# Optimization experiments

Hardware: AMD Instinct MI355X
Metric: run time of the kernel (lower is better)

## Reference

```python
import jax, jax.numpy as jnp
import numpy as np

FT_SIZE = 512
NUM_BUCKETS = 8
HID = 32
IN_FEATS = 770

def _crelu(x):
    return jnp.clip(x, 0.0, 1.0)

def setup_inputs() -> dict:
    key = jax.random.key(0)
    ks = jax.random.split(key, 8)
    B = 65536
    x = jax.random.uniform(ks[0], (B, 2 * IN_FEATS), dtype=jnp.float32)
    s = 0.05
    ft_w = jax.random.normal(ks[1], (FT_SIZE, IN_FEATS), dtype=jnp.float32) * s
    ft_b = jax.random.normal(ks[2], (FT_SIZE,), dtype=jnp.float32) * s
    h1_w = jax.random.normal(ks[3], (NUM_BUCKETS, HID, 2 * FT_SIZE), dtype=jnp.float32) * s
    h1_b = jax.random.normal(ks[4], (NUM_BUCKETS, HID), dtype=jnp.float32) * s
    h2_w = jax.random.normal(ks[5], (NUM_BUCKETS, HID, HID), dtype=jnp.float32) * s
    h2_b = jax.random.normal(ks[6], (NUM_BUCKETS, HID), dtype=jnp.float32) * s
    h3_w = jax.random.normal(ks[7], (NUM_BUCKETS, 1, HID), dtype=jnp.float32) * s
    h3_b = jnp.zeros((NUM_BUCKETS, 1), dtype=jnp.float32)
    return {"x": x, "ft_w": ft_w, "ft_b": ft_b, "h1_w": h1_w, "h1_b": h1_b,
            "h2_w": h2_w, "h2_b": h2_b, "h3_w": h3_w, "h3_b": h3_b}

def reference(x, ft_w, ft_b, h1_w, h1_b, h2_w, h2_b, h3_w, h3_b):
    stm = x[:, :IN_FEATS]          # [B, 770]
    nstm = x[:, IN_FEATS:]         # [B, 770]
    stm_ft = _crelu(stm @ ft_w.T + ft_b)    # [B, FT]
    nstm_ft = _crelu(nstm @ ft_w.T + ft_b)  # [B, FT]
    combined = jnp.concatenate([stm_ft, nstm_ft], axis=1)  # [B, 2FT]
    # bucket index from piece count (STM first 768 channels)
    pc = jnp.sum(x[:, :768], axis=1)
    bucket_idx = jnp.clip((pc * NUM_BUCKETS / 33.0).astype(jnp.int32), 0, NUM_BUCKETS - 1)  # [B]
    # compute all bucket heads (dense compute-all, matching original loop+stack)
    h = _crelu(jnp.einsum('bi,koi->bko', combined, h1_w) + h1_b)  # [B, K, 32]
    h = _crelu(jnp.einsum('bko,kpo->bkp', h, h2_w) + h2_b)        # [B, K, 32]
    all_out = jnp.einsum('bko,kpo->bkp', h, h3_w) + h3_b          # [B, K, 1]
    out = jnp.take_along_axis(all_out, bucket_idx[:, None, None], axis=1)  # [B,1,1]
    return out[:, 0, :]  # [B, 1]
```

## Files before the change

kernel.cpp:

```cpp
#include <hip/hip_runtime.h>
#include <hip/hip_bf16.h>
#include <stdint.h>


#define INF 770
#define KP  800
#define FT  512
#define K2  1024
#define N2  256

typedef _Float16 half8 __attribute__((ext_vector_type(8)));
typedef float floatx4 __attribute__((ext_vector_type(4)));

__device__ __forceinline__ float crelu_f(float v) {
    return v < 0.f ? 0.f : (v > 1.f ? 1.f : v);
}

__device__ __forceinline__ void gl_lds16(const _Float16* g, _Float16* l) {
    __builtin_amdgcn_global_load_lds(
        (__attribute__((address_space(1))) void*)(uintptr_t)(const void*)g,
        (__attribute__((address_space(3))) void*)l,
        16, 0, 0);
}

__global__ __launch_bounds__(256) void convert_x_kernel(
    const float* __restrict__ x, _Float16* __restrict__ x16,
    int* __restrict__ bucket, int B)
{
    __shared__ float red[4];
    int b = blockIdx.x;
    int tid = threadIdx.x, lane = tid & 63, w = tid >> 6;
    const float* src = x + (size_t)b * (2 * INF);
    _Float16* d0 = x16 + (size_t)b * KP;
    _Float16* d1 = x16 + ((size_t)B + b) * KP;
    float s = 0.f;
    for (int i = tid; i < KP; i += 256) {
        float v0 = 0.f, v1 = 0.f;
        if (i < INF) { v0 = src[i]; v1 = src[INF + i]; }
        d0[i] = (_Float16)v0;
        d1[i] = (_Float16)v1;
        if (i < 768) s += v0;
    }
    #pragma unroll
    for (int off = 32; off; off >>= 1) s += __shfl_down(s, off, 64);
    if (lane == 0) red[w] = s;
    __syncthreads();
    if (tid == 0) {
        float pc = red[0] + red[1] + red[2] + red[3];
        int bk = (int)(pc * (8.0f / 33.0f));
        bucket[b] = bk < 0 ? 0 : (bk > 7 ? 7 : bk);
    }
}

__global__ __launch_bounds__(256) void convert_w_kernel(
    const float* __restrict__ ftw, const float* __restrict__ h1w,
    _Float16* __restrict__ ftw16, _Float16* __restrict__ h1w16)
{
    int idx = blockIdx.x * 256 + threadIdx.x;
    const int FTW = FT * KP;
    if (idx < FTW) {
        int r = idx / KP, c = idx - r * KP;
        ftw16[idx] = (_Float16)(c < INF ? ftw[r * INF + c] : 0.f);
    } else {
        int j = idx - FTW;
        if (j < N2 * K2) h1w16[j] = (_Float16)h1w[j];
    }
}

__global__ __launch_bounds__(256) void gemm_ft_kernel(
    const _Float16* __restrict__ A,
    const _Float16* __restrict__ Bt,
    const float* __restrict__ bias,
    _Float16* __restrict__ C)
{
    __shared__ _Float16 lsA[128 * 32];
    __shared__ _Float16 lsB[128 * 32];
    int bid = blockIdx.x;
    int mt = bid >> 2, nt = bid & 3;
    int m0 = mt * 128, n0 = nt * 128;
    int tid = threadIdx.x, lane = tid & 63, w = tid >> 6;
    int rm = (w & 1) * 64, rn = (w >> 1) * 64;
    int colL = lane & 15, rowQ = lane >> 4;

    floatx4 acc[4][4] = {};

    for (int kt = 0; kt < KP / 32; ++kt) {
        int ks = kt * 32;
        #pragma unroll
        for (int p = 0; p < 2; ++p) {
            int qb = p * 256 + w * 64;
            int q = qb + lane;
            int r = q >> 2, c8 = q & 3;
            gl_lds16(A + (size_t)(m0 + r) * KP + ks + c8 * 8, lsA + qb * 8);
            gl_lds16(Bt + (size_t)(n0 + r) * KP + ks + c8 * 8, lsB + qb * 8);
        }
        asm volatile("s_waitcnt vmcnt(0)" ::: "memory");
        __syncthreads();

        half8 af[4], bf[4];
        #pragma unroll
        for (int i = 0; i < 4; ++i)
            af[i] = *(const half8*)(lsA + (rm + i * 16 + colL) * 32 + rowQ * 8);
        #pragma unroll
        for (int j = 0; j < 4; ++j)
            bf[j] = *(const half8*)(lsB + (rn + j * 16 + colL) * 32 + rowQ * 8);
        #pragma unroll
        for (int i = 0; i < 4; ++i)
            #pragma unroll
            for (int j = 0; j < 4; ++j)
                acc[i][j] = __builtin_amdgcn_mfma_f32_16x16x32_f16(af[i], bf[j], acc[i][j], 0, 0, 0);
        __syncthreads();
    }

    #pragma unroll
    for (int j = 0; j < 4; ++j) {
        int gn = n0 + rn + j * 16 + colL;
        float bv = bias[gn];
        #pragma unroll
        for (int i = 0; i < 4; ++i) {
            #pragma unroll
            for (int r = 0; r < 4; ++r) {
                int gm = m0 + rm + i * 16 + rowQ * 4 + r;
                float v = crelu_f(acc[i][j][r] + bv);
                C[(size_t)gm * FT + gn] = (_Float16)v;
            }
        }
    }
}

__global__ __launch_bounds__(256) void gemm_h1_kernel(
    const _Float16* __restrict__ C1,
    const _Float16* __restrict__ Bt,
    const float* __restrict__ bias,
    float* __restrict__ H,
    int B)
{
    __shared__ _Float16 lsA[128 * 32];
    __shared__ _Float16 lsB[128 * 32];
    int bid = blockIdx.x;
    int mt = bid >> 1, nt = bid & 1;
    int m0 = mt * 128, n0 = nt * 128;
    int tid = threadIdx.x, lane = tid & 63, w = tid >> 6;
    int rm = (w & 1) * 64, rn = (w >> 1) * 64;
    int colL = lane & 15, rowQ = lane >> 4;

    floatx4 acc[4][4] = {};

    for (int kt = 0; kt < K2 / 32; ++kt) {
        int ks = kt * 32;
        const _Float16* Abase = (ks < FT) ? (C1 + ks)
                                          : (C1 + (size_t)B * FT + (ks - FT));
        #pragma unroll
        for (int p = 0; p < 2; ++p) {
            int qb = p * 256 + w * 64;
            int q = qb + lane;
            int r = q >> 2, c8 = q & 3;
            gl_lds16(Abase + (size_t)(m0 + r) * FT + c8 * 8, lsA + qb * 8);
            gl_lds16(Bt + (size_t)(n0 + r) * K2 + ks + c8 * 8, lsB + qb * 8);
        }
        asm volatile("s_waitcnt vmcnt(0)" ::: "memory");
        __syncthreads();

        half8 af[4], bf[4];
        #pragma unroll
        for (int i = 0; i < 4; ++i)
            af[i] = *(const half8*)(lsA + (rm + i * 16 + colL) * 32 + rowQ * 8);
        #pragma unroll
        for (int j = 0; j < 4; ++j)
            bf[j] = *(const half8*)(lsB + (rn + j * 16 + colL) * 32 + rowQ * 8);
        #pragma unroll
        for (int i = 0; i < 4; ++i)
            #pragma unroll
            for (int j = 0; j < 4; ++j)
                acc[i][j] = __builtin_amdgcn_mfma_f32_16x16x32_f16(af[i], bf[j], acc[i][j], 0, 0, 0);
        __syncthreads();
    }

    #pragma unroll
    for (int j = 0; j < 4; ++j) {
        int gn = n0 + rn + j * 16 + colL;
        float bv = bias[gn];
        #pragma unroll
        for (int i = 0; i < 4; ++i) {
            #pragma unroll
            for (int r = 0; r < 4; ++r) {
                int gm = m0 + rm + i * 16 + rowQ * 4 + r;
                H[(size_t)gm * N2 + gn] = crelu_f(acc[i][j][r] + bv);
            }
        }
    }
}

__global__ __launch_bounds__(256) void tail_kernel(
    const float* __restrict__ H,
    const int* __restrict__ bucket,
    const float* __restrict__ h2w,
    const float* __restrict__ h2b,
    const float* __restrict__ h3w,
    const float* __restrict__ h3b,
    float* __restrict__ out, int B)
{
    int s = blockIdx.x * 8 + (threadIdx.x >> 5);
    int j = threadIdx.x & 31;
    if (s >= B) return;
    int k = bucket[s];
    float h1v = H[(size_t)s * N2 + k * 32 + j];
    const float* w2 = h2w + ((k * 32 + j) * 32);
    float a = h2b[k * 32 + j];
    #pragma unroll
    for (int i = 0; i < 32; ++i) a += w2[i] * __shfl(h1v, i, 32);
    a = crelu_f(a);
    float p = a * h3w[k * 32 + j];
    #pragma unroll
    for (int off = 16; off; off >>= 1) p += __shfl_down(p, off, 32);
    if (j == 0) out[s] = p + h3b[k];
}

extern "C" void kernel_launch(void* const* d_in, const int* in_sizes, int n_in,
                              void* d_out, int out_size, void* d_ws, size_t ws_size,
                              hipStream_t stream) {
    const float* x    = (const float*)d_in[0];
    const float* ftw  = (const float*)d_in[1];
    const float* ftb  = (const float*)d_in[2];
    const float* h1w  = (const float*)d_in[3];
    const float* h1b  = (const float*)d_in[4];
    const float* h2w  = (const float*)d_in[5];
    const float* h2b  = (const float*)d_in[6];
    const float* h3w  = (const float*)d_in[7];
    const float* h3b  = (const float*)d_in[8];
    float* out = (float*)d_out;

    int B = in_sizes[0] / (2 * INF);

    char* ws = (char*)d_ws;
    _Float16* x16   = (_Float16*)ws;
    size_t x16_b    = (size_t)2 * B * KP * sizeof(_Float16);
    _Float16* C1    = (_Float16*)(ws + x16_b);
    size_t c1_b     = (size_t)2 * B * FT * sizeof(_Float16);
    _Float16* ftw16 = (_Float16*)(ws + x16_b + c1_b);
    _Float16* h1w16 = ftw16 + (size_t)FT * KP;
    int* bucket     = (int*)(h1w16 + (size_t)N2 * K2);
    float* H        = (float*)ws;

    {
        int total = FT * KP + N2 * K2;
        convert_w_kernel<<<(total + 255) / 256, 256, 0, stream>>>(ftw, h1w, ftw16, h1w16);
    }
    convert_x_kernel<<<B, 256, 0, stream>>>(x, x16, bucket, B);
    {
        int grid = (2 * B / 128) * 4;
        gemm_ft_kernel<<<grid, 256, 0, stream>>>(x16, ftw16, ftb, C1);
    }
    {
        int grid = (B / 128) * 2;
        gemm_h1_kernel<<<grid, 256, 0, stream>>>(C1, h1w16, h1b, H, B);
    }
    tail_kernel<<<(B + 7) / 8, 256, 0, stream>>>(H, bucket, h2w, h2b, h3w, h3b, out, B);
}
```

Baseline: 898.2 us.

## Restructure FT and H1 GEMMs with LDS-resident B, register-prefetched A, XCD-aware mapping

```diff
diff --git a/kernel.cpp b/kernel.cpp
--- a/kernel.cpp
+++ b/kernel.cpp
@@ -3,14 +3,17 @@
 #include <stdint.h>
 
 
-#define INF 770
-#define KP  800
-#define FT  512
-#define K2  1024
-#define N2  256
+#define INF  770
+#define XROW 1540
+#define KP   800
+#define FT   512
+#define K2   1024
+#define N2   256
 
 typedef _Float16 half8 __attribute__((ext_vector_type(8)));
+typedef _Float16 half4 __attribute__((ext_vector_type(4)));
 typedef float floatx4 __attribute__((ext_vector_type(4)));
+typedef float floatx2 __attribute__((ext_vector_type(2)));
 
 __device__ __forceinline__ float crelu_f(float v) {
     return v < 0.f ? 0.f : (v > 1.f ? 1.f : v);
@@ -30,16 +33,30 @@
     __shared__ float red[4];
     int b = blockIdx.x;
     int tid = threadIdx.x, lane = tid & 63, w = tid >> 6;
-    const float* src = x + (size_t)b * (2 * INF);
-    _Float16* d0 = x16 + (size_t)b * KP;
-    _Float16* d1 = x16 + ((size_t)B + b) * KP;
+    const float* src = x + (size_t)b * XROW;
     float s = 0.f;
-    for (int i = tid; i < KP; i += 256) {
-        float v0 = 0.f, v1 = 0.f;
-        if (i < INF) { v0 = src[i]; v1 = src[INF + i]; }
-        d0[i] = (_Float16)v0;
-        d1[i] = (_Float16)v1;
-        if (i < 768) s += v0;
+    if (tid < 200) {
+        int i0 = tid * 4;
+        half4 v0, v1;
+        if (tid < 192) {
+            floatx4 f = *(const floatx4*)(src + i0);
+            v0[0] = (_Float16)f.x; v0[1] = (_Float16)f.y;
+            v0[2] = (_Float16)f.z; v0[3] = (_Float16)f.w;
+            s = (f.x + f.y) + (f.z + f.w);
+            floatx2 g0 = *(const floatx2*)(src + 770 + i0);
+            floatx2 g1 = *(const floatx2*)(src + 772 + i0);
+            v1[0] = (_Float16)g0.x; v1[1] = (_Float16)g0.y;
+            v1[2] = (_Float16)g1.x; v1[3] = (_Float16)g1.y;
+        } else if (tid == 192) {
+            floatx2 f = *(const floatx2*)(src + 768);
+            v0[0] = (_Float16)f.x; v0[1] = (_Float16)f.y; v0[2] = 0; v0[3] = 0;
+            floatx2 g = *(const floatx2*)(src + 1538);
+            v1[0] = (_Float16)g.x; v1[1] = (_Float16)g.y; v1[2] = 0; v1[3] = 0;
+        } else {
+            v0 = half4{0, 0, 0, 0}; v1 = half4{0, 0, 0, 0};
+        }
+        *(half4*)(x16 + (size_t)b * KP + i0) = v0;
+        *(half4*)(x16 + ((size_t)B + b) * KP + i0) = v1;
     }
     #pragma unroll
     for (int off = 32; off; off >>= 1) s += __shfl_down(s, off, 64);
@@ -47,7 +64,7 @@
     __syncthreads();
     if (tid == 0) {
         float pc = red[0] + red[1] + red[2] + red[3];
-        int bk = (int)(pc * (8.0f / 33.0f));
+        int bk = (int)((pc * 8.0f) / 33.0f);
         bucket[b] = bk < 0 ? 0 : (bk > 7 ? 7 : bk);
     }
 }
@@ -67,127 +84,170 @@
     }
 }
 
-__global__ __launch_bounds__(256) void gemm_ft_kernel(
+__global__ __launch_bounds__(256) void gemm_ft(
     const _Float16* __restrict__ A,
     const _Float16* __restrict__ Bt,
     const float* __restrict__ bias,
     _Float16* __restrict__ C)
 {
-    __shared__ _Float16 lsA[128 * 32];
-    __shared__ _Float16 lsB[128 * 32];
+    __shared__ _Float16 lsB[13 * 64 * 32];
     int bid = blockIdx.x;
-    int mt = bid >> 2, nt = bid & 3;
-    int m0 = mt * 128, n0 = nt * 128;
+    int xcd = bid & 7, kk = bid >> 3;
+    int mt = xcd * 64 + (kk >> 3), nt = kk & 7;
+    int m0 = mt * 256, n0 = nt * 64;
     int tid = threadIdx.x, lane = tid & 63, w = tid >> 6;
-    int rm = (w & 1) * 64, rn = (w >> 1) * 64;
     int colL = lane & 15, rowQ = lane >> 4;
+    int chA = rowQ ^ ((colL >> 1) & 3);
+    int mw = m0 + w * 64;
+
+    const _Float16* a0 = A + (size_t)(mw + colL) * KP + rowQ * 8;
 
     floatx4 acc[4][4] = {};
-
-    for (int kt = 0; kt < KP / 32; ++kt) {
-        int ks = kt * 32;
-        #pragma unroll
-        for (int p = 0; p < 2; ++p) {
-            int qb = p * 256 + w * 64;
-            int q = qb + lane;
-            int r = q >> 2, c8 = q & 3;
-            gl_lds16(A + (size_t)(m0 + r) * KP + ks + c8 * 8, lsA + qb * 8);
-            gl_lds16(Bt + (size_t)(n0 + r) * KP + ks + c8 * 8, lsB + qb * 8);
-        }
-        asm volatile("s_waitcnt vmcnt(0)" ::: "memory");
-        __syncthreads();
-
-        half8 af[4], bf[4];
-        #pragma unroll
-        for (int i = 0; i < 4; ++i)
-            af[i] = *(const half8*)(lsA + (rm + i * 16 + colL) * 32 + rowQ * 8);
+    half8 apf[3][4];
+
+    for (int t = tid; t < 13 * 256; t += 256) {
+        int ktb = t >> 8, r = t & 255, n = r >> 2, kq = r & 3;
+        int srcq = kq ^ ((n >> 1) & 3);
+        gl_lds16(Bt + (size_t)(n0 + n) * KP + ktb * 32 + srcq * 8, lsB + t * 8);
+    }
+    #pragma unroll
+    for (int d = 0; d < 3; ++d)
+        #pragma unroll
+        for (int i = 0; i < 4; ++i)
+            apf[d][i] = *(const half8*)(a0 + (size_t)i * 16 * KP + d * 32);
+    asm volatile("s_waitcnt vmcnt(0)" ::: "memory");
+    __syncthreads();
+
+    #pragma unroll
+    for (int kt = 0; kt < 25; ++kt) {
+        if (kt == 13) {
+            __syncthreads();
+            for (int t = tid; t < 12 * 256; t += 256) {
+                int ktb = t >> 8, r = t & 255, n = r >> 2, kq = r & 3;
+                int srcq = kq ^ ((n >> 1) & 3);
+                gl_lds16(Bt + (size_t)(n0 + n) * KP + (13 + ktb) * 32 + srcq * 8,
+                         lsB + t * 8);
+            }
+            asm volatile("s_waitcnt vmcnt(0)" ::: "memory");
+            __syncthreads();
+        }
+        int ktRel = (kt < 13) ? kt : kt - 13;
+        half8 bf[4], af[4];
         #pragma unroll
         for (int j = 0; j < 4; ++j)
-            bf[j] = *(const half8*)(lsB + (rn + j * 16 + colL) * 32 + rowQ * 8);
+            bf[j] = *(const half8*)(lsB + ktRel * 2048 + (j * 16 + colL) * 32 + chA * 8);
+        #pragma unroll
+        for (int i = 0; i < 4; ++i) af[i] = apf[kt % 3][i];
+        if (kt + 3 < 25) {
+            #pragma unroll
+            for (int i = 0; i < 4; ++i)
+                apf[kt % 3][i] = *(const half8*)(a0 + (size_t)i * 16 * KP + (kt + 3) * 32);
+        }
         #pragma unroll
         for (int i = 0; i < 4; ++i)
             #pragma unroll
             for (int j = 0; j < 4; ++j)
                 acc[i][j] = __builtin_amdgcn_mfma_f32_16x16x32_f16(af[i], bf[j], acc[i][j], 0, 0, 0);
-        __syncthreads();
     }
 
     #pragma unroll
     for (int j = 0; j < 4; ++j) {
-        int gn = n0 + rn + j * 16 + colL;
+        int gn = n0 + j * 16 + colL;
         float bv = bias[gn];
         #pragma unroll
-        for (int i = 0; i < 4; ++i) {
+        for (int i = 0; i < 4; ++i)
             #pragma unroll
             for (int r = 0; r < 4; ++r) {
-                int gm = m0 + rm + i * 16 + rowQ * 4 + r;
-                float v = crelu_f(acc[i][j][r] + bv);
-                C[(size_t)gm * FT + gn] = (_Float16)v;
+                int gm = mw + i * 16 + rowQ * 4 + r;
+                C[(size_t)gm * FT + gn] = (_Float16)crelu_f(acc[i][j][r] + bv);
             }
-        }
-    }
-}
-
-__global__ __launch_bounds__(256) void gemm_h1_kernel(
+    }
+}
+
+__global__ __launch_bounds__(256) void gemm_h1(
     const _Float16* __restrict__ C1,
     const _Float16* __restrict__ Bt,
     const float* __restrict__ bias,
     float* __restrict__ H,
     int B)
 {
-    __shared__ _Float16 lsA[128 * 32];
-    __shared__ _Float16 lsB[128 * 32];
+    __shared__ _Float16 lsB[13 * 64 * 32];
     int bid = blockIdx.x;
-    int mt = bid >> 1, nt = bid & 1;
-    int m0 = mt * 128, n0 = nt * 128;
+    int xcd = bid & 7, kk = bid >> 3;
+    int mt = xcd * 32 + (kk >> 2), nt = kk & 3;
+    int m0 = mt * 256, n0 = nt * 64;
     int tid = threadIdx.x, lane = tid & 63, w = tid >> 6;
-    int rm = (w & 1) * 64, rn = (w >> 1) * 64;
     int colL = lane & 15, rowQ = lane >> 4;
+    int chA = rowQ ^ ((colL >> 1) & 3);
+    int mw = m0 + w * 64;
+
+    const _Float16* a0lo = C1 + (size_t)(mw + colL) * FT + rowQ * 8;
+    const _Float16* a0hi = C1 + (size_t)(B + mw + colL) * FT + rowQ * 8;
 
     floatx4 acc[4][4] = {};
-
-    for (int kt = 0; kt < K2 / 32; ++kt) {
-        int ks = kt * 32;
-        const _Float16* Abase = (ks < FT) ? (C1 + ks)
-                                          : (C1 + (size_t)B * FT + (ks - FT));
-        #pragma unroll
-        for (int p = 0; p < 2; ++p) {
-            int qb = p * 256 + w * 64;
-            int q = qb + lane;
-            int r = q >> 2, c8 = q & 3;
-            gl_lds16(Abase + (size_t)(m0 + r) * FT + c8 * 8, lsA + qb * 8);
-            gl_lds16(Bt + (size_t)(n0 + r) * K2 + ks + c8 * 8, lsB + qb * 8);
-        }
-        asm volatile("s_waitcnt vmcnt(0)" ::: "memory");
-        __syncthreads();
-
-        half8 af[4], bf[4];
-        #pragma unroll
-        for (int i = 0; i < 4; ++i)
-            af[i] = *(const half8*)(lsA + (rm + i * 16 + colL) * 32 + rowQ * 8);
+    half8 apf[3][4];
+
+    #define H1_AFRAG(KT, I) \
+        (*(const half8*)(((KT) < 16 ? a0lo + (KT) * 32 : a0hi + ((KT) - 16) * 32) \
+                         + (size_t)(I) * 16 * FT))
+    #define H1_STAGE(KT0, NKT) do {                                             \
+        for (int t = tid; t < (NKT) * 256; t += 256) {                          \
+            int ktb = t >> 8, r = t & 255, n = r >> 2, kq = r & 3;              \
+            int srcq = kq ^ ((n >> 1) & 3);                                     \
+            gl_lds16(Bt + (size_t)(n0 + n) * K2 + ((KT0) + ktb) * 32 + srcq * 8,\
+                     lsB + t * 8);                                              \
+        }                                                                       \
+    } while (0)
+
+    H1_STAGE(0, 13);
+    #pragma unroll
+    for (int d = 0; d < 3; ++d)
+        #pragma unroll
+        for (int i = 0; i < 4; ++i)
+            apf[d][i] = H1_AFRAG(d, i);
+    asm volatile("s_waitcnt vmcnt(0)" ::: "memory");
+    __syncthreads();
+
+    #pragma unroll
+    for (int kt = 0; kt < 32; ++kt) {
+        if (kt == 13 || kt == 26) {
+            __syncthreads();
+            if (kt == 13) H1_STAGE(13, 13); else H1_STAGE(26, 6);
+            asm volatile("s_waitcnt vmcnt(0)" ::: "memory");
+            __syncthreads();
+        }
+        int ktRel = (kt < 13) ? kt : (kt < 26 ? kt - 13 : kt - 26);
+        half8 bf[4], af[4];
         #pragma unroll
         for (int j = 0; j < 4; ++j)
-            bf[j] = *(const half8*)(lsB + (rn + j * 16 + colL) * 32 + rowQ * 8);
+            bf[j] = *(const half8*)(lsB + ktRel * 2048 + (j * 16 + colL) * 32 + chA * 8);
+        #pragma unroll
+        for (int i = 0; i < 4; ++i) af[i] = apf[kt % 3][i];
+        if (kt + 3 < 32) {
+            #pragma unroll
+            for (int i = 0; i < 4; ++i)
+                apf[kt % 3][i] = H1_AFRAG(kt + 3, i);
+        }
         #pragma unroll
         for (int i = 0; i < 4; ++i)
             #pragma unroll
             for (int j = 0; j < 4; ++j)
                 acc[i][j] = __builtin_amdgcn_mfma_f32_16x16x32_f16(af[i], bf[j], acc[i][j], 0, 0, 0);
-        __syncthreads();
-    }
+    }
+    #undef H1_AFRAG
+    #undef H1_STAGE
 
     #pragma unroll
     for (int j = 0; j < 4; ++j) {
-        int gn = n0 + rn + j * 16 + colL;
+        int gn = n0 + j * 16 + colL;
         float bv = bias[gn];
         #pragma unroll
-        for (int i = 0; i < 4; ++i) {
+        for (int i = 0; i < 4; ++i)
             #pragma unroll
             for (int r = 0; r < 4; ++r) {
-                int gm = m0 + rm + i * 16 + rowQ * 4 + r;
+                int gm = mw + i * 16 + rowQ * 4 + r;
                 H[(size_t)gm * N2 + gn] = crelu_f(acc[i][j][r] + bv);
             }
-        }
     }
 }
 
@@ -238,8 +298,10 @@
     _Float16* C1    = (_Float16*)(ws + x16_b);
     size_t c1_b     = (size_t)2 * B * FT * sizeof(_Float16);
     _Float16* ftw16 = (_Float16*)(ws + x16_b + c1_b);
-    _Float16* h1w16 = ftw16 + (size_t)FT * KP;
-    int* bucket     = (int*)(h1w16 + (size_t)N2 * K2);
+    size_t ftw_b    = (size_t)FT * KP * sizeof(_Float16);
+    _Float16* h1w16 = (_Float16*)(ws + x16_b + c1_b + ftw_b);
+    size_t h1w_b    = (size_t)N2 * K2 * sizeof(_Float16);
+    int* bucket     = (int*)(ws + x16_b + c1_b + ftw_b + h1w_b);
     float* H        = (float*)ws;
 
     {
@@ -247,13 +309,7 @@
         convert_w_kernel<<<(total + 255) / 256, 256, 0, stream>>>(ftw, h1w, ftw16, h1w16);
     }
     convert_x_kernel<<<B, 256, 0, stream>>>(x, x16, bucket, B);
-    {
-        int grid = (2 * B / 128) * 4;
-        gemm_ft_kernel<<<grid, 256, 0, stream>>>(x16, ftw16, ftb, C1);
-    }
-    {
-        int grid = (B / 128) * 2;
-        gemm_h1_kernel<<<grid, 256, 0, stream>>>(C1, h1w16, h1b, H, B);
-    }
+    gemm_ft<<<4096, 256, 0, stream>>>(x16, ftw16, ftb, C1);
+    gemm_h1<<<1024, 256, 0, stream>>>(C1, h1w16, h1b, H, B);
     tail_kernel<<<(B + 7) / 8, 256, 0, stream>>>(H, bucket, h2w, h2b, h3w, h3b, out, B);
 }
```

Result: slower. 938.3 us (+4.5%).
